# Optimization experiments

Measured on AMD Instinct MI355X. Metric: run time of the kernel, lower is better.

Reference implementation:

```python
import jax, jax.numpy as jnp
import numpy as np
from jax import lax

B, T, L = 128, 4096, 64
START_ID, STOP_ID = 62, 63
NEG_INF = -10000.0


def setup_inputs() -> dict:
    key = jax.random.key(0)
    k1, k2 = jax.random.split(key)
    feats = jax.random.normal(k1, (B, T, L), dtype=jnp.float32)
    transitions = jax.random.normal(k2, (L, L), dtype=jnp.float32)
    # replicate the __init__ masking of start/stop transitions
    transitions = transitions.at[START_ID, :].set(NEG_INF)
    transitions = transitions.at[:, STOP_ID].set(NEG_INF)
    return {"feats": feats, "transitions": transitions}


def reference(feats, transitions):
    """Viterbi decode: returns (max log-likelihood score [B], best path [B, T])."""
    b, t_len, n_lab = feats.shape
    # log_delta[b, j]: best score ending in label j at current timestep
    log_delta0 = jnp.full((b, n_lab), NEG_INF, dtype=feats.dtype).at[:, START_ID].set(0.0)

    feats_t = jnp.swapaxes(feats, 0, 1)  # [T, B, L]

    def fwd_step(log_delta, feat_t):
        # m[b, i, j] = transitions[i, j] + log_delta[b, j]  (score of j -> i)
        m = transitions[None, :, :] + log_delta[:, None, :]  # [B, L, L]
        psi_t = jnp.argmax(m, axis=-1)                       # [B, L] backpointers
        log_delta = jnp.max(m, axis=-1) + feat_t             # [B, L]
        return log_delta, psi_t

    log_delta_T, psis = lax.scan(fwd_step, log_delta0, feats_t[1:])  # psis: [T-1, B, L]

    score = jnp.max(log_delta_T, axis=-1)        # [B]
    last_label = jnp.argmax(log_delta_T, axis=-1)  # [B]

    def back_step(next_label, psi_t):
        prev = jnp.take_along_axis(psi_t, next_label[:, None], axis=1)[:, 0]
        return prev, prev

    # psis[k] holds backpointers for timestep k+1; path[t] = psis[t][path[t+1]]
    _, path_prefix = lax.scan(back_step, last_label, psis, reverse=True)  # [T-1, B]
    path = jnp.concatenate([path_prefix.T, last_label[:, None]], axis=1)  # [B, T]
    return score, path
```

## Files before the change

kernel.cpp:

```cpp
#include <hip/hip_runtime.h>

constexpr int kB = 128;
constexpr int kT = 4096;
constexpr int kL = 64;
constexpr int kSeg = 64;
constexpr int kSegLen = 64;
constexpr float kNeg = -10000.0f;

typedef float f32x4 __attribute__((ext_vector_type(4)));

#if __has_builtin(__builtin_amdgcn_permlane16_swap)
#define HAS_PL16 1
#else
#define HAS_PL16 0
#endif

__device__ __forceinline__ float part4(const float (&tr)[16], const f32x4* dlp) {
  f32x4 v[4];
#pragma unroll
  for (int q = 0; q < 4; ++q) v[q] = dlp[q];
  float m[4];
#pragma unroll
  for (int q = 0; q < 4; ++q) {
    float a0 = tr[4 * q + 0] + v[q].x;
    float a1 = tr[4 * q + 1] + v[q].y;
    float a2 = tr[4 * q + 2] + v[q].z;
    float a3 = tr[4 * q + 3] + v[q].w;
    m[q] = fmaxf(fmaxf(fmaxf(a0, a1), a2), a3);
  }
  float part = fmaxf(fmaxf(fmaxf(m[0], m[1]), m[2]), m[3]);
  auto w2 = __builtin_amdgcn_permlane32_swap(__float_as_uint(part),
                                             __float_as_uint(part), false, false);
  return fmaxf(__uint_as_float(w2[0]), __uint_as_float(w2[1]));
}

__device__ __forceinline__ float step_shfl(const float (&tr)[16], const f32x4* dlp,
                                           float fo) {
  float m1 = part4(tr, dlp);
  return fmaxf(m1, __shfl_xor(m1, 16, 64)) + fo;
}

#if HAS_PL16
__device__ __forceinline__ float step_pl16(const float (&tr)[16], const f32x4* dlp,
                                           float fo) {
  float m1 = part4(tr, dlp);
  auto w2 = __builtin_amdgcn_permlane16_swap(__float_as_uint(m1),
                                             __float_as_uint(m1), false, false);
  return fmaxf(__uint_as_float(w2[0]), __uint_as_float(w2[1])) + fo;
}
#endif

__global__ __launch_bounds__(256, 1) void fwd_delta(const float* __restrict__ feats,
                                                    const float* __restrict__ trans,
                                                    float* __restrict__ delta) {
  const int tid = threadIdx.x;
  const int w = tid >> 6;
  const int lane = tid & 63;
  const int q = lane >> 4;
  const int li = lane & 15;
  const int o = 16 * w + li;
  const int b = blockIdx.x;
  const size_t kBL = (size_t)kB * kL;

  float tr[16];
#pragma unroll
  for (int k = 0; k < 16; k += 4) {
    float4 v = *reinterpret_cast<const float4*>(trans + o * kL + 16 * q + k);
    tr[k] = v.x; tr[k + 1] = v.y; tr[k + 2] = v.z; tr[k + 3] = v.w;
  }

  __shared__ __align__(16) float dbuf[2][kL];
  __shared__ int okf;
  const f32x4* dlp0 = reinterpret_cast<const f32x4*>(&dbuf[0][16 * q]);
  const f32x4* dlp1 = reinterpret_cast<const f32x4*>(&dbuf[1][16 * q]);

  if (tid == 0) okf = 1;
  if (tid < kL) {
    float dd = (tid == 62) ? 0.0f : kNeg;
    dbuf[0][tid] = dd;
    delta[(size_t)b * kL + tid] = dd;
  }
  __syncthreads();

  const float* fpo = feats + (size_t)b * kT * kL + o;
  float* dro = delta + (size_t)b * kL + o;

#define LDS_BAR()                                                               \
  {                                                                             \
    asm volatile("s_waitcnt lgkmcnt(0)" ::: "memory");                          \
    __builtin_amdgcn_s_barrier();                                               \
  }

  {
    float fA = fpo[64 * 1], fB = fpo[64 * 2];
    float d1 = step_shfl(tr, dlp0, fA);
    if (lane < 16) dbuf[1][o] = d1;
    LDS_BAR();
    float d2 = step_shfl(tr, dlp1, fB);
    LDS_BAR();
#if HAS_PL16
    float p1 = step_pl16(tr, dlp0, fA);
    if (lane < 16) dbuf[1][o] = p1;
    LDS_BAR();
    float p2 = step_pl16(tr, dlp1, fB);
    LDS_BAR();
    bool wok = __all((__float_as_int(p1) == __float_as_int(d1)) &&
                     (__float_as_int(p2) == __float_as_int(d2))) != 0;
    if (!wok && lane == 0) okf = 0;
#else
    (void)d2;
    if (lane == 0) okf = 0;
#endif
    __syncthreads();
  }
  const bool use16 = (okf != 0);

  float f0 = fpo[64 * 1], f1 = fpo[64 * 2], f2 = fpo[64 * 3], f3 = fpo[64 * 4];
  const float* pf = fpo + 64 * 5;
  size_t off = kBL;

#define STEP(FN, DLP, WBUF, FV)                                                 \
  {                                                                             \
    float dnew = FN(tr, DLP, FV);                                               \
    if (lane < 16) {                                                            \
      dbuf[WBUF][o] = dnew;                                                     \
      dro[off] = dnew;                                                          \
    }                                                                           \
    off += kBL;                                                                 \
    LDS_BAR();                                                                  \
  }

#if HAS_PL16
  if (use16) {
    for (int it = 0; it < 1022; ++it) {
      STEP(step_pl16, dlp0, 1, f0) f0 = pf[0];
      STEP(step_pl16, dlp1, 0, f1) f1 = pf[64];
      STEP(step_pl16, dlp0, 1, f2) f2 = pf[128];
      STEP(step_pl16, dlp1, 0, f3) f3 = pf[192];
      pf += 256;
    }
    float g0 = pf[0], g1 = pf[64], g2 = pf[128];
    STEP(step_pl16, dlp0, 1, f0)
    STEP(step_pl16, dlp1, 0, f1)
    STEP(step_pl16, dlp0, 1, f2)
    STEP(step_pl16, dlp1, 0, f3)
    STEP(step_pl16, dlp0, 1, g0)
    STEP(step_pl16, dlp1, 0, g1)
    STEP(step_pl16, dlp0, 1, g2)
  } else
#endif
  {
    for (int it = 0; it < 1022; ++it) {
      STEP(step_shfl, dlp0, 1, f0) f0 = pf[0];
      STEP(step_shfl, dlp1, 0, f1) f1 = pf[64];
      STEP(step_shfl, dlp0, 1, f2) f2 = pf[128];
      STEP(step_shfl, dlp1, 0, f3) f3 = pf[192];
      pf += 256;
    }
    float g0 = pf[0], g1 = pf[64], g2 = pf[128];
    STEP(step_shfl, dlp0, 1, f0)
    STEP(step_shfl, dlp1, 0, f1)
    STEP(step_shfl, dlp0, 1, f2)
    STEP(step_shfl, dlp1, 0, f3)
    STEP(step_shfl, dlp0, 1, g0)
    STEP(step_shfl, dlp1, 0, g1)
    STEP(step_shfl, dlp0, 1, g2)
  }
#undef STEP
#undef LDS_BAR
}

__global__ __launch_bounds__(256) void psi_from_delta(const float* __restrict__ delta,
                                                      const float* __restrict__ trans,
                                                      unsigned char* __restrict__ psi) {
  const int lane = threadIdx.x & 63;
  const int w = __builtin_amdgcn_readfirstlane(blockIdx.x * 4 + (threadIdx.x >> 6));
  float tr[kL];
#pragma unroll
  for (int k = 0; k < kL; k += 4) {
    float4 v = *reinterpret_cast<const float4*>(trans + lane * kL + k);
    tr[k] = v.x; tr[k + 1] = v.y; tr[k + 2] = v.z; tr[k + 3] = v.w;
  }
  const int r0 = w * 8;
  for (int rr = 0; rr < 8; ++rr) {
    const int r = r0 + rr;
    const float4* row4 = reinterpret_cast<const float4*>(delta + (size_t)r * kL);
    float bA = -INFINITY, bBv = -INFINITY;
    int iA = 0, iB = 32;
#pragma unroll
    for (int q = 0; q < 8; ++q) {
      float4 dv = row4[q];
      float c; bool g;
      c = tr[4 * q + 0] + dv.x; g = c > bA; bA = g ? c : bA; iA = g ? 4 * q + 0 : iA;
      c = tr[4 * q + 1] + dv.y; g = c > bA; bA = g ? c : bA; iA = g ? 4 * q + 1 : iA;
      c = tr[4 * q + 2] + dv.z; g = c > bA; bA = g ? c : bA; iA = g ? 4 * q + 2 : iA;
      c = tr[4 * q + 3] + dv.w; g = c > bA; bA = g ? c : bA; iA = g ? 4 * q + 3 : iA;
    }
#pragma unroll
    for (int q = 8; q < 16; ++q) {
      float4 dv = row4[q];
      float c; bool g;
      c = tr[4 * q + 0] + dv.x; g = c > bBv; bBv = g ? c : bBv; iB = g ? 4 * q + 0 : iB;
      c = tr[4 * q + 1] + dv.y; g = c > bBv; bBv = g ? c : bBv; iB = g ? 4 * q + 1 : iB;
      c = tr[4 * q + 2] + dv.z; g = c > bBv; bBv = g ? c : bBv; iB = g ? 4 * q + 2 : iB;
      c = tr[4 * q + 3] + dv.w; g = c > bBv; bBv = g ? c : bBv; iB = g ? 4 * q + 3 : iB;
    }
    bool gm = bBv > bA;
    psi[(size_t)r * kL + lane] = (unsigned char)(gm ? iB : iA);
  }
}

__global__ __launch_bounds__(256) void seg_compose(unsigned char* psiM,
                                                   unsigned char* __restrict__ C) {
  const int lane = threadIdx.x & 63;
  const int w = blockIdx.x * 4 + (threadIdx.x >> 6);
  const int s = w >> 7;
  const int b = w & 127;
  const int tstart = s * kSegLen;
  const int tend = (tstart + kSegLen < kT) ? tstart + kSegLen : kT - 1;
  const size_t stride = (size_t)kB * kL;
  size_t off = ((size_t)(tend - 1) * kB + b) * kL + lane;
  int m = lane;
  int v = psiM[off];
  for (int t = tend - 1; t > tstart; --t) {
    int vn = psiM[off - stride];
    m = __shfl(v, m, 64);
    psiM[off] = (unsigned char)m;
    v = vn;
    off -= stride;
  }
  m = __shfl(v, m, 64);
  psiM[off] = (unsigned char)m;
  C[((size_t)s * kB + b) * kL + lane] = (unsigned char)m;
}

__global__ __launch_bounds__(64) void score_scan(const float* __restrict__ dfin,
                                                 const unsigned char* __restrict__ C,
                                                 int* __restrict__ E,
                                                 float* __restrict__ out) {
  const int b = blockIdx.x;
  const int i = threadIdx.x;
  float d = dfin[(size_t)b * kL + i];
  float m = d;
#pragma unroll
  for (int off = 32; off; off >>= 1) m = fmaxf(m, __shfl_xor(m, off, 64));
  unsigned long long msk = __ballot(d == m);
  int ll = __ffsll(msk) - 1;
  if (i == 0) {
    out[b] = m;
    out[kB + (size_t)b * kT + (kT - 1)] = (float)ll;
    int lbl = ll;
    for (int s = kSeg - 1; s >= 0; --s) {
      E[s * kB + b] = lbl;
      lbl = C[((size_t)s * kB + b) * kL + lbl];
    }
  }
}

__global__ __launch_bounds__(256) void path_fill(const unsigned char* __restrict__ M,
                                                 const int* __restrict__ E,
                                                 float* __restrict__ out) {
  const int n = blockIdx.x * 256 + threadIdx.x;
  const int b = n >> 12;
  const int t = n & (kT - 1);
  if (t == kT - 1) return;
  const int e = E[(t >> 6) * kB + b];
  const unsigned char lab = M[((size_t)t * kB + b) * kL + e];
  out[kB + (size_t)b * kT + t] = (float)lab;
}

extern "C" void kernel_launch(void* const* d_in, const int* in_sizes, int n_in,
                              void* d_out, int out_size, void* d_ws, size_t ws_size,
                              hipStream_t stream) {
  const float* feats = (const float*)d_in[0];
  const float* trans = (const float*)d_in[1];
  float* out = (float*)d_out;
  char* ws = (char*)d_ws;

  const size_t deltaB = (size_t)kT * kB * kL * 4;
  const size_t psiB   = (size_t)kT * kB * kL;
  const size_t CBy    = (size_t)kSeg * kB * kL;

  float* delta = (float*)ws;
  unsigned char* psi = (unsigned char*)(ws + deltaB);
  unsigned char* C = (unsigned char*)(ws + deltaB + psiB);
  int* E = (int*)(ws + deltaB + psiB + CBy);
  hipLaunchKernelGGL(fwd_delta, dim3(kB), dim3(256), 0, stream, feats, trans, delta);
  hipLaunchKernelGGL(psi_from_delta, dim3(16380), dim3(256), 0, stream, delta, trans, psi);
  hipLaunchKernelGGL(seg_compose, dim3(2048), dim3(256), 0, stream, psi, C);
  hipLaunchKernelGGL(score_scan, dim3(kB), dim3(64), 0, stream,
                     delta + (size_t)(kT - 1) * kB * kL, C, E, out);
  hipLaunchKernelGGL(path_fill, dim3(2048), dim3(256), 0, stream, psi, E, out);
}
```

Before: 1.018 ms.

## Split forward recurrence across 8 waves with 8-wide partial max per lane

New measurement: 1.094 ms. +7.5%, slower.

```diff
diff --git a/kernel.cpp b/kernel.cpp
--- a/kernel.cpp
+++ b/kernel.cpp
@@ -10,69 +10,73 @@
 typedef float f32x4 __attribute__((ext_vector_type(4)));
 
 #if __has_builtin(__builtin_amdgcn_permlane16_swap)
-#define HAS_PL16 1
+#define HAS_PLX 1
 #else
-#define HAS_PL16 0
-#endif
-
-__device__ __forceinline__ float part4(const float (&tr)[16], const f32x4* dlp) {
-  f32x4 v[4];
-#pragma unroll
-  for (int q = 0; q < 4; ++q) v[q] = dlp[q];
-  float m[4];
-#pragma unroll
-  for (int q = 0; q < 4; ++q) {
-    float a0 = tr[4 * q + 0] + v[q].x;
-    float a1 = tr[4 * q + 1] + v[q].y;
-    float a2 = tr[4 * q + 2] + v[q].z;
-    float a3 = tr[4 * q + 3] + v[q].w;
-    m[q] = fmaxf(fmaxf(fmaxf(a0, a1), a2), a3);
-  }
-  float part = fmaxf(fmaxf(fmaxf(m[0], m[1]), m[2]), m[3]);
-  auto w2 = __builtin_amdgcn_permlane32_swap(__float_as_uint(part),
-                                             __float_as_uint(part), false, false);
-  return fmaxf(__uint_as_float(w2[0]), __uint_as_float(w2[1]));
-}
-
-__device__ __forceinline__ float step_shfl(const float (&tr)[16], const f32x4* dlp,
-                                           float fo) {
-  float m1 = part4(tr, dlp);
-  return fmaxf(m1, __shfl_xor(m1, 16, 64)) + fo;
-}
-
-#if HAS_PL16
-__device__ __forceinline__ float step_pl16(const float (&tr)[16], const f32x4* dlp,
-                                           float fo) {
-  float m1 = part4(tr, dlp);
-  auto w2 = __builtin_amdgcn_permlane16_swap(__float_as_uint(m1),
-                                             __float_as_uint(m1), false, false);
-  return fmaxf(__uint_as_float(w2[0]), __uint_as_float(w2[1])) + fo;
-}
-#endif
-
-__global__ __launch_bounds__(256, 1) void fwd_delta(const float* __restrict__ feats,
+#define HAS_PLX 0
+#endif
+
+__device__ __forceinline__ float part8(const float (&tr)[8], const f32x4* dlp) {
+  f32x4 v0 = dlp[0], v1 = dlp[1];
+  float a0 = tr[0] + v0.x, a1 = tr[1] + v0.y;
+  float a2 = tr[2] + v0.z, a3 = tr[3] + v0.w;
+  float a4 = tr[4] + v1.x, a5 = tr[5] + v1.y;
+  float a6 = tr[6] + v1.z, a7 = tr[7] + v1.w;
+  float m0 = fmaxf(fmaxf(a0, a1), a2);
+  float m1 = fmaxf(fmaxf(a3, a4), a5);
+  float m2 = fmaxf(a6, a7);
+  return fmaxf(fmaxf(m0, m1), m2);
+}
+
+__device__ __forceinline__ float step_shfl8(const float (&tr)[8], const f32x4* dlp,
+                                            float fo) {
+  float m = part8(tr, dlp);
+  m = fmaxf(m, __shfl_xor(m, 32, 64));
+  m = fmaxf(m, __shfl_xor(m, 16, 64));
+  m = fmaxf(m, __shfl_xor(m, 8, 64));
+  return m + fo;
+}
+
+#if HAS_PLX
+__device__ __forceinline__ float step_pl8(const float (&tr)[8], const f32x4* dlp,
+                                          float fo) {
+  float m = part8(tr, dlp);
+  auto w2 = __builtin_amdgcn_permlane32_swap(__float_as_uint(m), __float_as_uint(m),
+                                             false, false);
+  m = fmaxf(__uint_as_float(w2[0]), __uint_as_float(w2[1]));
+  auto w3 = __builtin_amdgcn_permlane16_swap(__float_as_uint(m), __float_as_uint(m),
+                                             false, false);
+  m = fmaxf(__uint_as_float(w3[0]), __uint_as_float(w3[1]));
+  int r = __builtin_amdgcn_update_dpp(0, __float_as_int(m), 0x128 ,
+                                      0xF, 0xF, true);
+  m = fmaxf(m, __int_as_float(r));
+  return m + fo;
+}
+#endif
+
+__global__ __launch_bounds__(512, 1) void fwd_delta(const float* __restrict__ feats,
                                                     const float* __restrict__ trans,
                                                     float* __restrict__ delta) {
   const int tid = threadIdx.x;
   const int w = tid >> 6;
   const int lane = tid & 63;
-  const int q = lane >> 4;
-  const int li = lane & 15;
-  const int o = 16 * w + li;
+  const int g = lane >> 3;
+  const int li = lane & 7;
+  const int o = 8 * w + li;
   const int b = blockIdx.x;
   const size_t kBL = (size_t)kB * kL;
 
-  float tr[16];
-#pragma unroll
-  for (int k = 0; k < 16; k += 4) {
-    float4 v = *reinterpret_cast<const float4*>(trans + o * kL + 16 * q + k);
-    tr[k] = v.x; tr[k + 1] = v.y; tr[k + 2] = v.z; tr[k + 3] = v.w;
+  float tr[8];
+  {
+    float4 v = *reinterpret_cast<const float4*>(trans + o * kL + 8 * g);
+    tr[0] = v.x; tr[1] = v.y; tr[2] = v.z; tr[3] = v.w;
+    float4 u = *reinterpret_cast<const float4*>(trans + o * kL + 8 * g + 4);
+    tr[4] = u.x; tr[5] = u.y; tr[6] = u.z; tr[7] = u.w;
   }
 
   __shared__ __align__(16) float dbuf[2][kL];
   __shared__ int okf;
-  const f32x4* dlp0 = reinterpret_cast<const f32x4*>(&dbuf[0][16 * q]);
-  const f32x4* dlp1 = reinterpret_cast<const f32x4*>(&dbuf[1][16 * q]);
+  const f32x4* dlp0 = reinterpret_cast<const f32x4*>(&dbuf[0][8 * g]);
+  const f32x4* dlp1 = reinterpret_cast<const f32x4*>(&dbuf[1][8 * g]);
 
   if (tid == 0) okf = 1;
   if (tid < kL) {
@@ -93,16 +97,16 @@
 
   {
     float fA = fpo[64 * 1], fB = fpo[64 * 2];
-    float d1 = step_shfl(tr, dlp0, fA);
-    if (lane < 16) dbuf[1][o] = d1;
-    LDS_BAR();
-    float d2 = step_shfl(tr, dlp1, fB);
-    LDS_BAR();
-#if HAS_PL16
-    float p1 = step_pl16(tr, dlp0, fA);
-    if (lane < 16) dbuf[1][o] = p1;
-    LDS_BAR();
-    float p2 = step_pl16(tr, dlp1, fB);
+    float d1 = step_shfl8(tr, dlp0, fA);
+    if (lane < 8) dbuf[1][o] = d1;
+    LDS_BAR();
+    float d2 = step_shfl8(tr, dlp1, fB);
+    LDS_BAR();
+#if HAS_PLX
+    float p1 = step_pl8(tr, dlp0, fA);
+    if (lane < 8) dbuf[1][o] = p1;
+    LDS_BAR();
+    float p2 = step_pl8(tr, dlp1, fB);
     LDS_BAR();
     bool wok = __all((__float_as_int(p1) == __float_as_int(d1)) &&
                      (__float_as_int(p2) == __float_as_int(d2))) != 0;
@@ -113,7 +117,7 @@
 #endif
     __syncthreads();
   }
-  const bool use16 = (okf != 0);
+  const bool use8 = (okf != 0);
 
   float f0 = fpo[64 * 1], f1 = fpo[64 * 2], f2 = fpo[64 * 3], f3 = fpo[64 * 4];
   const float* pf = fpo + 64 * 5;
@@ -122,7 +126,7 @@
 #define STEP(FN, DLP, WBUF, FV)                                                 \
   {                                                                             \
     float dnew = FN(tr, DLP, FV);                                               \
-    if (lane < 16) {                                                            \
+    if (lane < 8) {                                                             \
       dbuf[WBUF][o] = dnew;                                                     \
       dro[off] = dnew;                                                          \
     }                                                                           \
@@ -130,41 +134,41 @@
     LDS_BAR();                                                                  \
   }
 
-#if HAS_PL16
-  if (use16) {
+#if HAS_PLX
+  if (use8) {
     for (int it = 0; it < 1022; ++it) {
-      STEP(step_pl16, dlp0, 1, f0) f0 = pf[0];
-      STEP(step_pl16, dlp1, 0, f1) f1 = pf[64];
-      STEP(step_pl16, dlp0, 1, f2) f2 = pf[128];
-      STEP(step_pl16, dlp1, 0, f3) f3 = pf[192];
+      STEP(step_pl8, dlp0, 1, f0) f0 = pf[0];
+      STEP(step_pl8, dlp1, 0, f1) f1 = pf[64];
+      STEP(step_pl8, dlp0, 1, f2) f2 = pf[128];
+      STEP(step_pl8, dlp1, 0, f3) f3 = pf[192];
       pf += 256;
     }
     float g0 = pf[0], g1 = pf[64], g2 = pf[128];
-    STEP(step_pl16, dlp0, 1, f0)
-    STEP(step_pl16, dlp1, 0, f1)
-    STEP(step_pl16, dlp0, 1, f2)
-    STEP(step_pl16, dlp1, 0, f3)
-    STEP(step_pl16, dlp0, 1, g0)
-    STEP(step_pl16, dlp1, 0, g1)
-    STEP(step_pl16, dlp0, 1, g2)
+    STEP(step_pl8, dlp0, 1, f0)
+    STEP(step_pl8, dlp1, 0, f1)
+    STEP(step_pl8, dlp0, 1, f2)
+    STEP(step_pl8, dlp1, 0, f3)
+    STEP(step_pl8, dlp0, 1, g0)
+    STEP(step_pl8, dlp1, 0, g1)
+    STEP(step_pl8, dlp0, 1, g2)
   } else
 #endif
   {
     for (int it = 0; it < 1022; ++it) {
-      STEP(step_shfl, dlp0, 1, f0) f0 = pf[0];
-      STEP(step_shfl, dlp1, 0, f1) f1 = pf[64];
-      STEP(step_shfl, dlp0, 1, f2) f2 = pf[128];
-      STEP(step_shfl, dlp1, 0, f3) f3 = pf[192];
+      STEP(step_shfl8, dlp0, 1, f0) f0 = pf[0];
+      STEP(step_shfl8, dlp1, 0, f1) f1 = pf[64];
+      STEP(step_shfl8, dlp0, 1, f2) f2 = pf[128];
+      STEP(step_shfl8, dlp1, 0, f3) f3 = pf[192];
       pf += 256;
     }
     float g0 = pf[0], g1 = pf[64], g2 = pf[128];
-    STEP(step_shfl, dlp0, 1, f0)
-    STEP(step_shfl, dlp1, 0, f1)
-    STEP(step_shfl, dlp0, 1, f2)
-    STEP(step_shfl, dlp1, 0, f3)
-    STEP(step_shfl, dlp0, 1, g0)
-    STEP(step_shfl, dlp1, 0, g1)
-    STEP(step_shfl, dlp0, 1, g2)
+    STEP(step_shfl8, dlp0, 1, f0)
+    STEP(step_shfl8, dlp1, 0, f1)
+    STEP(step_shfl8, dlp0, 1, f2)
+    STEP(step_shfl8, dlp1, 0, f3)
+    STEP(step_shfl8, dlp0, 1, g0)
+    STEP(step_shfl8, dlp1, 0, g1)
+    STEP(step_shfl8, dlp0, 1, g2)
   }
 #undef STEP
 #undef LDS_BAR
@@ -285,7 +289,7 @@
   unsigned char* psi = (unsigned char*)(ws + deltaB);
   unsigned char* C = (unsigned char*)(ws + deltaB + psiB);
   int* E = (int*)(ws + deltaB + psiB + CBy);
-  hipLaunchKernelGGL(fwd_delta, dim3(kB), dim3(256), 0, stream, feats, trans, delta);
+  hipLaunchKernelGGL(fwd_delta, dim3(kB), dim3(512), 0, stream, feats, trans, delta);
   hipLaunchKernelGGL(psi_from_delta, dim3(16380), dim3(256), 0, stream, delta, trans, psi);
   hipLaunchKernelGGL(seg_compose, dim3(2048), dim3(256), 0, stream, psi, C);
   hipLaunchKernelGGL(score_scan, dim3(kB), dim3(64), 0, stream,
```

## Store forward max values and find backpointers by equality match

Applied to the files above, without the earlier changes.

New measurement: 1.195 ms. 1.17x slower.

```diff
diff --git a/kernel.cpp b/kernel.cpp
--- a/kernel.cpp
+++ b/kernel.cpp
@@ -34,25 +34,25 @@
   return fmaxf(__uint_as_float(w2[0]), __uint_as_float(w2[1]));
 }
 
-__device__ __forceinline__ float step_shfl(const float (&tr)[16], const f32x4* dlp,
-                                           float fo) {
+__device__ __forceinline__ float red_shfl(const float (&tr)[16], const f32x4* dlp) {
   float m1 = part4(tr, dlp);
-  return fmaxf(m1, __shfl_xor(m1, 16, 64)) + fo;
+  return fmaxf(m1, __shfl_xor(m1, 16, 64));
 }
 
 #if HAS_PL16
-__device__ __forceinline__ float step_pl16(const float (&tr)[16], const f32x4* dlp,
-                                           float fo) {
+__device__ __forceinline__ float red_pl16(const float (&tr)[16], const f32x4* dlp) {
   float m1 = part4(tr, dlp);
   auto w2 = __builtin_amdgcn_permlane16_swap(__float_as_uint(m1),
                                              __float_as_uint(m1), false, false);
-  return fmaxf(__uint_as_float(w2[0]), __uint_as_float(w2[1])) + fo;
+  return fmaxf(__uint_as_float(w2[0]), __uint_as_float(w2[1]));
 }
 #endif
 
-__global__ __launch_bounds__(256, 1) void fwd_delta(const float* __restrict__ feats,
-                                                    const float* __restrict__ trans,
-                                                    float* __restrict__ delta) {
+template <bool MX>
+__global__ __launch_bounds__(256, 1) void fwd_delta_t(const float* __restrict__ feats,
+                                                      const float* __restrict__ trans,
+                                                      float* __restrict__ delta,
+                                                      float* __restrict__ mx) {
   const int tid = threadIdx.x;
   const int w = tid >> 6;
   const int lane = tid & 63;
@@ -84,6 +84,7 @@
 
   const float* fpo = feats + (size_t)b * kT * kL + o;
   float* dro = delta + (size_t)b * kL + o;
+  float* mxo = MX ? (mx + (size_t)b * kL + o) : nullptr;
 
 #define LDS_BAR()                                                               \
   {                                                                             \
@@ -93,16 +94,16 @@
 
   {
     float fA = fpo[64 * 1], fB = fpo[64 * 2];
-    float d1 = step_shfl(tr, dlp0, fA);
+    float d1 = red_shfl(tr, dlp0) + fA;
     if (lane < 16) dbuf[1][o] = d1;
     LDS_BAR();
-    float d2 = step_shfl(tr, dlp1, fB);
+    float d2 = red_shfl(tr, dlp1) + fB;
     LDS_BAR();
 #if HAS_PL16
-    float p1 = step_pl16(tr, dlp0, fA);
+    float p1 = red_pl16(tr, dlp0) + fA;
     if (lane < 16) dbuf[1][o] = p1;
     LDS_BAR();
-    float p2 = step_pl16(tr, dlp1, fB);
+    float p2 = red_pl16(tr, dlp1) + fB;
     LDS_BAR();
     bool wok = __all((__float_as_int(p1) == __float_as_int(d1)) &&
                      (__float_as_int(p2) == __float_as_int(d2))) != 0;
@@ -121,10 +122,12 @@
 
 #define STEP(FN, DLP, WBUF, FV)                                                 \
   {                                                                             \
-    float dnew = FN(tr, DLP, FV);                                               \
+    float m2v = FN(tr, DLP);                                                    \
+    float dnew = m2v + FV;                                                      \
     if (lane < 16) {                                                            \
       dbuf[WBUF][o] = dnew;                                                     \
       dro[off] = dnew;                                                          \
+      if (MX) mxo[off] = m2v;                                                   \
     }                                                                           \
     off += kBL;                                                                 \
     LDS_BAR();                                                                  \
@@ -133,41 +136,72 @@
 #if HAS_PL16
   if (use16) {
     for (int it = 0; it < 1022; ++it) {
-      STEP(step_pl16, dlp0, 1, f0) f0 = pf[0];
-      STEP(step_pl16, dlp1, 0, f1) f1 = pf[64];
-      STEP(step_pl16, dlp0, 1, f2) f2 = pf[128];
-      STEP(step_pl16, dlp1, 0, f3) f3 = pf[192];
+      STEP(red_pl16, dlp0, 1, f0) f0 = pf[0];
+      STEP(red_pl16, dlp1, 0, f1) f1 = pf[64];
+      STEP(red_pl16, dlp0, 1, f2) f2 = pf[128];
+      STEP(red_pl16, dlp1, 0, f3) f3 = pf[192];
       pf += 256;
     }
     float g0 = pf[0], g1 = pf[64], g2 = pf[128];
-    STEP(step_pl16, dlp0, 1, f0)
-    STEP(step_pl16, dlp1, 0, f1)
-    STEP(step_pl16, dlp0, 1, f2)
-    STEP(step_pl16, dlp1, 0, f3)
-    STEP(step_pl16, dlp0, 1, g0)
-    STEP(step_pl16, dlp1, 0, g1)
-    STEP(step_pl16, dlp0, 1, g2)
+    STEP(red_pl16, dlp0, 1, f0)
+    STEP(red_pl16, dlp1, 0, f1)
+    STEP(red_pl16, dlp0, 1, f2)
+    STEP(red_pl16, dlp1, 0, f3)
+    STEP(red_pl16, dlp0, 1, g0)
+    STEP(red_pl16, dlp1, 0, g1)
+    STEP(red_pl16, dlp0, 1, g2)
   } else
 #endif
   {
     for (int it = 0; it < 1022; ++it) {
-      STEP(step_shfl, dlp0, 1, f0) f0 = pf[0];
-      STEP(step_shfl, dlp1, 0, f1) f1 = pf[64];
-      STEP(step_shfl, dlp0, 1, f2) f2 = pf[128];
-      STEP(step_shfl, dlp1, 0, f3) f3 = pf[192];
+      STEP(red_shfl, dlp0, 1, f0) f0 = pf[0];
+      STEP(red_shfl, dlp1, 0, f1) f1 = pf[64];
+      STEP(red_shfl, dlp0, 1, f2) f2 = pf[128];
+      STEP(red_shfl, dlp1, 0, f3) f3 = pf[192];
       pf += 256;
     }
     float g0 = pf[0], g1 = pf[64], g2 = pf[128];
-    STEP(step_shfl, dlp0, 1, f0)
-    STEP(step_shfl, dlp1, 0, f1)
-    STEP(step_shfl, dlp0, 1, f2)
-    STEP(step_shfl, dlp1, 0, f3)
-    STEP(step_shfl, dlp0, 1, g0)
-    STEP(step_shfl, dlp1, 0, g1)
-    STEP(step_shfl, dlp0, 1, g2)
+    STEP(red_shfl, dlp0, 1, f0)
+    STEP(red_shfl, dlp1, 0, f1)
+    STEP(red_shfl, dlp0, 1, f2)
+    STEP(red_shfl, dlp1, 0, f3)
+    STEP(red_shfl, dlp0, 1, g0)
+    STEP(red_shfl, dlp1, 0, g1)
+    STEP(red_shfl, dlp0, 1, g2)
   }
 #undef STEP
 #undef LDS_BAR
+}
+
+__global__ __launch_bounds__(256) void psi_eq(const float* __restrict__ delta,
+                                              const float* __restrict__ mx,
+                                              const float* __restrict__ trans,
+                                              unsigned char* __restrict__ psi) {
+  const int lane = threadIdx.x & 63;
+  const int w = __builtin_amdgcn_readfirstlane(blockIdx.x * 4 + (threadIdx.x >> 6));
+  float tr[kL];
+#pragma unroll
+  for (int k = 0; k < kL; k += 4) {
+    float4 v = *reinterpret_cast<const float4*>(trans + lane * kL + k);
+    tr[k] = v.x; tr[k + 1] = v.y; tr[k + 2] = v.z; tr[k + 3] = v.w;
+  }
+  const int r0 = w * 8;
+  for (int rr = 0; rr < 8; ++rr) {
+    const int r = r0 + rr;
+    const float4* row4 = reinterpret_cast<const float4*>(delta + (size_t)r * kL);
+    const float target = mx[((size_t)r + kB) * kL + lane];
+    int idx = 0;
+#pragma unroll
+    for (int qq = 15; qq >= 0; --qq) {
+      float4 dv = row4[qq];
+      float c;
+      c = tr[4 * qq + 3] + dv.w; idx = (c == target) ? 4 * qq + 3 : idx;
+      c = tr[4 * qq + 2] + dv.z; idx = (c == target) ? 4 * qq + 2 : idx;
+      c = tr[4 * qq + 1] + dv.y; idx = (c == target) ? 4 * qq + 1 : idx;
+      c = tr[4 * qq + 0] + dv.x; idx = (c == target) ? 4 * qq + 0 : idx;
+    }
+    psi[(size_t)r * kL + lane] = (unsigned char)idx;
+  }
 }
 
 __global__ __launch_bounds__(256) void psi_from_delta(const float* __restrict__ delta,
@@ -278,15 +312,31 @@
   char* ws = (char*)d_ws;
 
   const size_t deltaB = (size_t)kT * kB * kL * 4;
+  const size_t mxB    = deltaB;
   const size_t psiB   = (size_t)kT * kB * kL;
   const size_t CBy    = (size_t)kSeg * kB * kL;
+  const size_t EBy    = (size_t)kSeg * kB * 4;
+
+  const bool bigws = ws_size >= deltaB + mxB + psiB + CBy + EBy;
 
   float* delta = (float*)ws;
-  unsigned char* psi = (unsigned char*)(ws + deltaB);
-  unsigned char* C = (unsigned char*)(ws + deltaB + psiB);
-  int* E = (int*)(ws + deltaB + psiB + CBy);
-  hipLaunchKernelGGL(fwd_delta, dim3(kB), dim3(256), 0, stream, feats, trans, delta);
-  hipLaunchKernelGGL(psi_from_delta, dim3(16380), dim3(256), 0, stream, delta, trans, psi);
+  float* mx = bigws ? (float*)(ws + deltaB) : nullptr;
+  char* base = ws + deltaB + (bigws ? mxB : 0);
+  unsigned char* psi = (unsigned char*)base;
+  unsigned char* C = (unsigned char*)(base + psiB);
+  int* E = (int*)(base + psiB + CBy);
+
+  if (bigws) {
+    hipLaunchKernelGGL(fwd_delta_t<true>, dim3(kB), dim3(256), 0, stream,
+                       feats, trans, delta, mx);
+    hipLaunchKernelGGL(psi_eq, dim3(16380), dim3(256), 0, stream,
+                       delta, mx, trans, psi);
+  } else {
+    hipLaunchKernelGGL(fwd_delta_t<false>, dim3(kB), dim3(256), 0, stream,
+                       feats, trans, delta, nullptr);
+    hipLaunchKernelGGL(psi_from_delta, dim3(16380), dim3(256), 0, stream,
+                       delta, trans, psi);
+  }
   hipLaunchKernelGGL(seg_compose, dim3(2048), dim3(256), 0, stream, psi, C);
   hipLaunchKernelGGL(score_scan, dim3(kB), dim3(64), 0, stream,
                      delta + (size_t)(kT - 1) * kB * kL, C, E, out);
```

## Fuse backpointer computation into forward Viterbi kernel via shared-memory delta ring

Applied to the files above, without the earlier changes.

Measured after the change: 1.561 ms. 53.3% more time.

```diff
diff --git a/kernel.cpp b/kernel.cpp
--- a/kernel.cpp
+++ b/kernel.cpp
@@ -34,179 +34,191 @@
   return fmaxf(__uint_as_float(w2[0]), __uint_as_float(w2[1]));
 }
 
-__device__ __forceinline__ float step_shfl(const float (&tr)[16], const f32x4* dlp,
-                                           float fo) {
+__device__ __forceinline__ float red_shfl(const float (&tr)[16], const f32x4* dlp) {
   float m1 = part4(tr, dlp);
-  return fmaxf(m1, __shfl_xor(m1, 16, 64)) + fo;
+  return fmaxf(m1, __shfl_xor(m1, 16, 64));
 }
 
 #if HAS_PL16
-__device__ __forceinline__ float step_pl16(const float (&tr)[16], const f32x4* dlp,
-                                           float fo) {
+__device__ __forceinline__ float red_pl16(const float (&tr)[16], const f32x4* dlp) {
   float m1 = part4(tr, dlp);
   auto w2 = __builtin_amdgcn_permlane16_swap(__float_as_uint(m1),
                                              __float_as_uint(m1), false, false);
-  return fmaxf(__uint_as_float(w2[0]), __uint_as_float(w2[1])) + fo;
-}
-#endif
-
-__global__ __launch_bounds__(256, 1) void fwd_delta(const float* __restrict__ feats,
-                                                    const float* __restrict__ trans,
-                                                    float* __restrict__ delta) {
-  const int tid = threadIdx.x;
-  const int w = tid >> 6;
-  const int lane = tid & 63;
-  const int q = lane >> 4;
-  const int li = lane & 15;
-  const int o = 16 * w + li;
-  const int b = blockIdx.x;
-  const size_t kBL = (size_t)kB * kL;
-
-  float tr[16];
-#pragma unroll
-  for (int k = 0; k < 16; k += 4) {
-    float4 v = *reinterpret_cast<const float4*>(trans + o * kL + 16 * q + k);
-    tr[k] = v.x; tr[k + 1] = v.y; tr[k + 2] = v.z; tr[k + 3] = v.w;
-  }
-
-  __shared__ __align__(16) float dbuf[2][kL];
-  __shared__ int okf;
-  const f32x4* dlp0 = reinterpret_cast<const f32x4*>(&dbuf[0][16 * q]);
-  const f32x4* dlp1 = reinterpret_cast<const f32x4*>(&dbuf[1][16 * q]);
-
-  if (tid == 0) okf = 1;
-  if (tid < kL) {
-    float dd = (tid == 62) ? 0.0f : kNeg;
-    dbuf[0][tid] = dd;
-    delta[(size_t)b * kL + tid] = dd;
-  }
-  __syncthreads();
-
-  const float* fpo = feats + (size_t)b * kT * kL + o;
-  float* dro = delta + (size_t)b * kL + o;
+  return fmaxf(__uint_as_float(w2[0]), __uint_as_float(w2[1]));
+}
+#endif
+
+__device__ __forceinline__ void psi_row(const float (&trp)[kL], const float* ringf,
+                                        int rt, int b, int label,
+                                        unsigned char* __restrict__ psi) {
+  if (rt < 0 || rt > kT - 2) return;
+  const f32x4* rp = reinterpret_cast<const f32x4*>(ringf + (rt & 15) * kL);
+  float best = -INFINITY;
+  int idx = 0;
+#pragma unroll
+  for (int qq = 0; qq < 16; ++qq) {
+    f32x4 v = rp[qq];
+    float c; bool g;
+    c = trp[4 * qq + 0] + v.x; g = c > best; best = g ? c : best; idx = g ? 4 * qq + 0 : idx;
+    c = trp[4 * qq + 1] + v.y; g = c > best; best = g ? c : best; idx = g ? 4 * qq + 1 : idx;
+    c = trp[4 * qq + 2] + v.z; g = c > best; best = g ? c : best; idx = g ? 4 * qq + 2 : idx;
+    c = trp[4 * qq + 3] + v.w; g = c > best; best = g ? c : best; idx = g ? 4 * qq + 3 : idx;
+  }
+  psi[((size_t)rt * kB + b) * kL + label] = (unsigned char)idx;
+}
 
 #define LDS_BAR()                                                               \
   {                                                                             \
     asm volatile("s_waitcnt lgkmcnt(0)" ::: "memory");                          \
     __builtin_amdgcn_s_barrier();                                               \
   }
-
-  {
-    float fA = fpo[64 * 1], fB = fpo[64 * 2];
-    float d1 = step_shfl(tr, dlp0, fA);
-    if (lane < 16) dbuf[1][o] = d1;
-    LDS_BAR();
-    float d2 = step_shfl(tr, dlp1, fB);
-    LDS_BAR();
+#define BAR4() LDS_BAR() LDS_BAR() LDS_BAR() LDS_BAR()
+#define BAR8() BAR4() BAR4()
+
+__global__ __launch_bounds__(512, 1) void fwd_psi_fused(const float* __restrict__ feats,
+                                                        const float* __restrict__ trans,
+                                                        unsigned char* __restrict__ psi,
+                                                        float* __restrict__ dfin) {
+  const int tid = threadIdx.x;
+  const int wv = tid >> 6;
+  const int lane = tid & 63;
+  const int b = blockIdx.x;
+
+  __shared__ __align__(16) float ring[16][kL];
+  __shared__ int okf;
+  float* ringf = &ring[0][0];
+
+  if (tid == 0) okf = 1;
+  if (tid < kL) ring[0][tid] = (tid == 62) ? 0.0f : kNeg;
+  __syncthreads();
+
+  if (wv < 4) {
+    const int q = lane >> 4;
+    const int li = lane & 15;
+    const int o = 16 * wv + li;
+    const bool li16 = (lane < 16);
+    float tr[16];
+#pragma unroll
+    for (int k = 0; k < 16; k += 4) {
+      float4 v = *reinterpret_cast<const float4*>(trans + o * kL + 16 * q + k);
+      tr[k] = v.x; tr[k + 1] = v.y; tr[k + 2] = v.z; tr[k + 3] = v.w;
+    }
+    const float* bq16f = ringf + 16 * q;
+    const float* fpo = feats + (size_t)b * kT * kL + o;
+
+    {
+      float fA = fpo[64 * 1], fB = fpo[64 * 2];
+      float d1 = red_shfl(tr, (const f32x4*)(bq16f + 0 * kL)) + fA;
+      if (li16) ringf[1 * kL + o] = d1;
+      LDS_BAR();
+      float d2 = red_shfl(tr, (const f32x4*)(bq16f + 1 * kL)) + fB;
+      LDS_BAR();
 #if HAS_PL16
-    float p1 = step_pl16(tr, dlp0, fA);
-    if (lane < 16) dbuf[1][o] = p1;
-    LDS_BAR();
-    float p2 = step_pl16(tr, dlp1, fB);
-    LDS_BAR();
-    bool wok = __all((__float_as_int(p1) == __float_as_int(d1)) &&
-                     (__float_as_int(p2) == __float_as_int(d2))) != 0;
-    if (!wok && lane == 0) okf = 0;
+      float p1 = red_pl16(tr, (const f32x4*)(bq16f + 0 * kL)) + fA;
+      if (li16) ringf[1 * kL + o] = p1;
+      LDS_BAR();
+      float p2 = red_pl16(tr, (const f32x4*)(bq16f + 1 * kL)) + fB;
+      LDS_BAR();
+      bool wok = __all((__float_as_int(p1) == __float_as_int(d1)) &&
+                       (__float_as_int(p2) == __float_as_int(d2))) != 0;
+      if (!wok && lane == 0) okf = 0;
 #else
-    (void)d2;
-    if (lane == 0) okf = 0;
+      (void)d2;
+      if (lane == 0) okf = 0;
+#endif
+      __syncthreads();
+    }
+    const bool use16 = (okf != 0);
+
+    float dlast = 0.0f;
+    float f0 = fpo[64 * 1], f1 = fpo[64 * 2], f2 = fpo[64 * 3], f3 = fpo[64 * 4];
+    float f4 = fpo[64 * 5], f5 = fpo[64 * 6], f6 = fpo[64 * 7], f7 = fpo[64 * 8];
+    float f8 = fpo[64 * 9], f9 = fpo[64 * 10], f10 = fpo[64 * 11], f11 = fpo[64 * 12];
+    float f12 = fpo[64 * 13], f13 = fpo[64 * 14], f14 = fpo[64 * 15], f15 = fpo[64 * 16];
+    const float* pf = fpo + 64 * 17;
+
+#define FSTEP(FN, RS, WS, FV)                                                   \
+    {                                                                           \
+      float m2v = FN(tr, (const f32x4*)(bq16f + (RS) * kL));                    \
+      dlast = m2v + FV;                                                         \
+      if (li16) ringf[(WS) * kL + o] = dlast;                                   \
+      LDS_BAR();                                                                \
+    }
+#define FITER(FN)                                                               \
+    {                                                                           \
+      FSTEP(FN, 0, 1, f0)   f0 = pf[0];                                         \
+      FSTEP(FN, 1, 2, f1)   f1 = pf[64];                                        \
+      FSTEP(FN, 2, 3, f2)   f2 = pf[128];                                       \
+      FSTEP(FN, 3, 4, f3)   f3 = pf[192];                                       \
+      FSTEP(FN, 4, 5, f4)   f4 = pf[256];                                       \
+      FSTEP(FN, 5, 6, f5)   f5 = pf[320];                                       \
+      FSTEP(FN, 6, 7, f6)   f6 = pf[384];                                       \
+      FSTEP(FN, 7, 8, f7)   f7 = pf[448];                                       \
+      FSTEP(FN, 8, 9, f8)   f8 = pf[512];                                       \
+      FSTEP(FN, 9, 10, f9)  f9 = pf[576];                                       \
+      FSTEP(FN, 10, 11, f10) f10 = pf[640];                                     \
+      FSTEP(FN, 11, 12, f11) f11 = pf[704];                                     \
+      FSTEP(FN, 12, 13, f12) f12 = pf[768];                                     \
+      FSTEP(FN, 13, 14, f13) f13 = pf[832];                                     \
+      FSTEP(FN, 14, 15, f14) f14 = pf[896];                                     \
+      FSTEP(FN, 15, 0, f15)  f15 = pf[(it == 254) ? 896 : 960];                 \
+      pf += 1024;                                                               \
+    }
+#define FEPI(FN)                                                                \
+    {                                                                           \
+      FSTEP(FN, 0, 1, f0)   FSTEP(FN, 1, 2, f1)   FSTEP(FN, 2, 3, f2)           \
+      FSTEP(FN, 3, 4, f3)   FSTEP(FN, 4, 5, f4)   FSTEP(FN, 5, 6, f5)           \
+      FSTEP(FN, 6, 7, f6)   FSTEP(FN, 7, 8, f7)   FSTEP(FN, 8, 9, f8)           \
+      FSTEP(FN, 9, 10, f9)  FSTEP(FN, 10, 11, f10) FSTEP(FN, 11, 12, f11)       \
+      FSTEP(FN, 12, 13, f12) FSTEP(FN, 13, 14, f13) FSTEP(FN, 14, 15, f14)      \
+    }
+
+#if HAS_PL16
+    if (use16) {
+      for (int it = 0; it < 255; ++it) FITER(red_pl16)
+      FEPI(red_pl16)
+    } else
+#endif
+    {
+      for (int it = 0; it < 255; ++it) FITER(red_shfl)
+      FEPI(red_shfl)
+    }
+#undef FEPI
+#undef FITER
+#undef FSTEP
+    if (li16) dfin[(size_t)b * kL + o] = dlast;
+  } else {
+    const int pw = wv - 4;
+    const int label = lane;
+    float trp[kL];
+#pragma unroll
+    for (int k = 0; k < kL; k += 4) {
+      float4 v = *reinterpret_cast<const float4*>(trans + label * kL + k);
+      trp[k] = v.x; trp[k + 1] = v.y; trp[k + 2] = v.z; trp[k + 3] = v.w;
+    }
+    LDS_BAR() LDS_BAR()
+#if HAS_PL16
+    LDS_BAR() LDS_BAR()
 #endif
     __syncthreads();
-  }
-  const bool use16 = (okf != 0);
-
-  float f0 = fpo[64 * 1], f1 = fpo[64 * 2], f2 = fpo[64 * 3], f3 = fpo[64 * 4];
-  const float* pf = fpo + 64 * 5;
-  size_t off = kBL;
-
-#define STEP(FN, DLP, WBUF, FV)                                                 \
-  {                                                                             \
-    float dnew = FN(tr, DLP, FV);                                               \
-    if (lane < 16) {                                                            \
-      dbuf[WBUF][o] = dnew;                                                     \
-      dro[off] = dnew;                                                          \
-    }                                                                           \
-    off += kBL;                                                                 \
-    LDS_BAR();                                                                  \
-  }
-
-#if HAS_PL16
-  if (use16) {
-    for (int it = 0; it < 1022; ++it) {
-      STEP(step_pl16, dlp0, 1, f0) f0 = pf[0];
-      STEP(step_pl16, dlp1, 0, f1) f1 = pf[64];
-      STEP(step_pl16, dlp0, 1, f2) f2 = pf[128];
-      STEP(step_pl16, dlp1, 0, f3) f3 = pf[192];
-      pf += 256;
-    }
-    float g0 = pf[0], g1 = pf[64], g2 = pf[128];
-    STEP(step_pl16, dlp0, 1, f0)
-    STEP(step_pl16, dlp1, 0, f1)
-    STEP(step_pl16, dlp0, 1, f2)
-    STEP(step_pl16, dlp1, 0, f3)
-    STEP(step_pl16, dlp0, 1, g0)
-    STEP(step_pl16, dlp1, 0, g1)
-    STEP(step_pl16, dlp0, 1, g2)
-  } else
-#endif
-  {
-    for (int it = 0; it < 1022; ++it) {
-      STEP(step_shfl, dlp0, 1, f0) f0 = pf[0];
-      STEP(step_shfl, dlp1, 0, f1) f1 = pf[64];
-      STEP(step_shfl, dlp0, 1, f2) f2 = pf[128];
-      STEP(step_shfl, dlp1, 0, f3) f3 = pf[192];
-      pf += 256;
-    }
-    float g0 = pf[0], g1 = pf[64], g2 = pf[128];
-    STEP(step_shfl, dlp0, 1, f0)
-    STEP(step_shfl, dlp1, 0, f1)
-    STEP(step_shfl, dlp0, 1, f2)
-    STEP(step_shfl, dlp1, 0, f3)
-    STEP(step_shfl, dlp0, 1, g0)
-    STEP(step_shfl, dlp1, 0, g1)
-    STEP(step_shfl, dlp0, 1, g2)
-  }
-#undef STEP
-#undef LDS_BAR
-}
-
-__global__ __launch_bounds__(256) void psi_from_delta(const float* __restrict__ delta,
-                                                      const float* __restrict__ trans,
-                                                      unsigned char* __restrict__ psi) {
-  const int lane = threadIdx.x & 63;
-  const int w = __builtin_amdgcn_readfirstlane(blockIdx.x * 4 + (threadIdx.x >> 6));
-  float tr[kL];
-#pragma unroll
-  for (int k = 0; k < kL; k += 4) {
-    float4 v = *reinterpret_cast<const float4*>(trans + lane * kL + k);
-    tr[k] = v.x; tr[k + 1] = v.y; tr[k + 2] = v.z; tr[k + 3] = v.w;
-  }
-  const int r0 = w * 8;
-  for (int rr = 0; rr < 8; ++rr) {
-    const int r = r0 + rr;
-    const float4* row4 = reinterpret_cast<const float4*>(delta + (size_t)r * kL);
-    float bA = -INFINITY, bBv = -INFINITY;
-    int iA = 0, iB = 32;
-#pragma unroll
-    for (int q = 0; q < 8; ++q) {
-      float4 dv = row4[q];
-      float c; bool g;
-      c = tr[4 * q + 0] + dv.x; g = c > bA; bA = g ? c : bA; iA = g ? 4 * q + 0 : iA;
-      c = tr[4 * q + 1] + dv.y; g = c > bA; bA = g ? c : bA; iA = g ? 4 * q + 1 : iA;
-      c = tr[4 * q + 2] + dv.z; g = c > bA; bA = g ? c : bA; iA = g ? 4 * q + 2 : iA;
-      c = tr[4 * q + 3] + dv.w; g = c > bA; bA = g ? c : bA; iA = g ? 4 * q + 3 : iA;
-    }
-#pragma unroll
-    for (int q = 8; q < 16; ++q) {
-      float4 dv = row4[q];
-      float c; bool g;
-      c = tr[4 * q + 0] + dv.x; g = c > bBv; bBv = g ? c : bBv; iB = g ? 4 * q + 0 : iB;
-      c = tr[4 * q + 1] + dv.y; g = c > bBv; bBv = g ? c : bBv; iB = g ? 4 * q + 1 : iB;
-      c = tr[4 * q + 2] + dv.z; g = c > bBv; bBv = g ? c : bBv; iB = g ? 4 * q + 2 : iB;
-      c = tr[4 * q + 3] + dv.w; g = c > bBv; bBv = g ? c : bBv; iB = g ? 4 * q + 3 : iB;
-    }
-    bool gm = bBv > bA;
-    psi[(size_t)r * kL + lane] = (unsigned char)(gm ? iB : iA);
+
+#define PSI2(BASE)                                                              \
+    {                                                                           \
+      psi_row(trp, ringf, (BASE) + 2 * pw, b, label, psi);                      \
+      psi_row(trp, ringf, (BASE) + 2 * pw + 1, b, label, psi);                  \
+    }
+    for (int it = 0; it < 255; ++it) {
+      PSI2(16 * it - 7)
+      BAR8()
+      PSI2(16 * it + 1)
+      BAR8()
+    }
+    PSI2(4073)
+    BAR8()
+    PSI2(4081)
+    BAR4() LDS_BAR() LDS_BAR() LDS_BAR()
+    PSI2(4089)
+#undef PSI2
   }
 }
 
@@ -277,18 +289,18 @@
   float* out = (float*)d_out;
   char* ws = (char*)d_ws;
 
-  const size_t deltaB = (size_t)kT * kB * kL * 4;
-  const size_t psiB   = (size_t)kT * kB * kL;
-  const size_t CBy    = (size_t)kSeg * kB * kL;
-
-  float* delta = (float*)ws;
-  unsigned char* psi = (unsigned char*)(ws + deltaB);
-  unsigned char* C = (unsigned char*)(ws + deltaB + psiB);
-  int* E = (int*)(ws + deltaB + psiB + CBy);
-  hipLaunchKernelGGL(fwd_delta, dim3(kB), dim3(256), 0, stream, feats, trans, delta);
-  hipLaunchKernelGGL(psi_from_delta, dim3(16380), dim3(256), 0, stream, delta, trans, psi);
+  const size_t psiB = (size_t)kT * kB * kL;
+  const size_t CBy  = (size_t)kSeg * kB * kL;
+  const size_t EBy  = (size_t)kSeg * kB * 4;
+
+  unsigned char* psi = (unsigned char*)ws;
+  unsigned char* C = (unsigned char*)(ws + psiB);
+  int* E = (int*)(ws + psiB + CBy);
+  float* dfin = (float*)(ws + psiB + CBy + EBy);
+
+  hipLaunchKernelGGL(fwd_psi_fused, dim3(kB), dim3(512), 0, stream,
+                     feats, trans, psi, dfin);
   hipLaunchKernelGGL(seg_compose, dim3(2048), dim3(256), 0, stream, psi, C);
-  hipLaunchKernelGGL(score_scan, dim3(kB), dim3(64), 0, stream,
-                     delta + (size_t)(kT - 1) * kB * kL, C, E, out);
+  hipLaunchKernelGGL(score_scan, dim3(kB), dim3(64), 0, stream, dfin, C, E, out);
   hipLaunchKernelGGL(path_fill, dim3(2048), dim3(256), 0, stream, psi, E, out);
 }
```
